# Optimization experiments

Hardware: AMD Instinct MI355X
Metric: run time of the kernel (lower is better)

## Reference

```python
import jax, jax.numpy as jnp
import numpy as np

T = 36          # temporal length (dictionary rows)
NP = 161        # number of atoms = 1 + 80 + 80
LAMBDA = 0.005
MAX_ITER = 100
EPS = 1e-10
STOP_TOL = 1e-5


def setup_inputs() -> dict:
    key = jax.random.key(0)
    k1, k2, k3 = jax.random.split(key, 3)
    y = jax.random.normal(k1, (4096, T, 50), dtype=jnp.float32)
    r = jax.random.uniform(k2, (80,), dtype=jnp.float32)      # pole magnitudes
    theta = jax.random.uniform(k3, (80,), dtype=jnp.float32)  # pole phases
    return {"y": y, "r": r, "theta": theta}


def build_dictionary(r, theta):
    # D[i,:] = [1+eps, r^i*cos(i*theta), r^i*sin(i*theta)], column-normalized
    i = jnp.arange(T, dtype=r.dtype)[:, None]          # [T,1]
    r_pow = r[None, :] ** i                            # [T,80]
    ang = i * theta[None, :]                           # [T,80]
    one_col = jnp.full((T, 1), 1.0 + EPS, dtype=r.dtype)
    D = jnp.concatenate([one_col, r_pow * jnp.cos(ang), r_pow * jnp.sin(ang)], axis=1)  # [T,NP]
    D = D / jnp.linalg.norm(D, axis=0, keepdims=True)
    return D


def fista_reweighted(D, Y, lambd, w):
    # D: [T,NP], Y: [N,T,M], w: [N,NP,M]
    DtD = D.T @ D                                       # [NP,NP]
    DtY = jnp.einsum('tp,ntm->npm', D, Y)               # [N,NP,M]
    L = jnp.linalg.norm(DtD, ord=2)                     # spectral norm
    Linv = 1.0 / L
    weighted_lambd = w * lambd * Linv
    A = jnp.eye(NP, dtype=D.dtype) - DtD * Linv         # [NP,NP]
    const_xminus = DtY * Linv - weighted_lambd
    const_xplus = DtY * Linv + weighted_lambd
    x0 = jnp.zeros_like(DtY)

    def step(carry, _):
        x_old, y_old, t_old, done = carry
        Ay = jnp.einsum('pq,nqm->npm', A, y_old)
        x_new = jnp.maximum(0.0, Ay + const_xminus) + jnp.minimum(0.0, Ay + const_xplus)
        t_new = (1.0 + jnp.sqrt(1.0 + 4.0 * t_old ** 2)) / 2.0
        tt = (t_old - 1.0) / t_new
        y_new = x_new + tt * (x_new - x_old)
        # early-stop check (divisor NP == x_old.shape[1] for full-shaped x)
        cnv = jnp.linalg.norm((x_old - x_new).ravel()) / NP < STOP_TOL
        x_out = jnp.where(done, x_old, x_new)
        y_out = jnp.where(done, y_old, y_new)
        t_out = jnp.where(done, t_old, t_new)
        return (x_out, y_out, t_out, done | cnv), None

    init = (x0, x0, jnp.asarray(1.0, D.dtype), jnp.asarray(False))
    (x_final, _, _, _), _ = jax.lax.scan(step, init, None, length=MAX_ITER)
    return x_final


def reference(y, r, theta):
    D = build_dictionary(r, theta)                      # [T,NP], normalized
    w = jnp.ones((y.shape[0], NP, y.shape[2]), dtype=y.dtype)
    C_pred = fista_reweighted(D, y, LAMBDA, w)          # [N,NP,M]
    Y_pred = jnp.einsum('tp,npm->ntm', D, C_pred)       # [N,T,M]
    return (Y_pred, C_pred)
```

## Files before the change

kernel.cpp:

```cpp
#include <hip/hip_runtime.h>

#define T36   36
#define NPAR  161
#define MM    50
#define NN    4096
#define NCOLS (NN*MM)
#define MP    48
#define KP    192
#define KV    64
#define CB    32
#define YPITCH 200
#define VPITCH 72

typedef _Float16 half8 __attribute__((ext_vector_type(8)));
typedef _Float16 half4 __attribute__((ext_vector_type(4)));
typedef float    f32x4 __attribute__((ext_vector_type(4)));

#define MFMA16(a,b,c) __builtin_amdgcn_mfma_f32_16x16x32_f16(a,b,c,0,0,0)

__device__ float g_D[MP*KP];
__device__ float g_DT[KP*KV];
__device__ float g_sc[2];

__global__ __launch_bounds__(256) void setup_kernel(const float* __restrict__ r,
                                                    const float* __restrict__ th) {
  __shared__ float Dl[MP][KP];
  __shared__ float El[T36][T36];
  __shared__ float Fl[T36][T36];
  __shared__ float Gl[T36][T36];
  __shared__ float vl[T36], v2[T36], v3[T36];
  __shared__ float sc;
  __shared__ int jmaxs;
  const int tid = threadIdx.x;

  for (int e = tid; e < MP*KP; e += 256) (&Dl[0][0])[e] = 0.0f;
  __syncthreads();

  if (tid < NPAR) {
    const int p = tid;
    float col[T36];
    if (p == 0) {
      #pragma unroll
      for (int t = 0; t < T36; ++t) col[t] = 1.0f;
    } else if (p <= 80) {
      const float a = r[p-1], w = th[p-1];
      for (int t = 0; t < T36; ++t) col[t] = powf(a, (float)t) * cosf((float)t * w);
    } else {
      const float a = r[p-81], w = th[p-81];
      for (int t = 0; t < T36; ++t) col[t] = powf(a, (float)t) * sinf((float)t * w);
    }
    float s = 0.0f;
    for (int t = 0; t < T36; ++t) s += col[t]*col[t];
    const float inv = 1.0f / sqrtf(s);
    for (int t = 0; t < T36; ++t) Dl[t][p] = col[t] * inv;
  }
  __syncthreads();

  for (int e = tid; e < MP*KP; e += 256) g_D[e] = (&Dl[0][0])[e];
  for (int e = tid; e < KP*KV; e += 256) {
    const int p = e / KV, t = e % KV;
    g_DT[e] = (t < MP) ? Dl[t][p] : 0.0f;
  }

  for (int e = tid; e < T36*T36; e += 256) {
    const int a = e / T36, b = e % T36;
    float s = 0.0f;
    for (int p = 0; p < KP; ++p) s += Dl[a][p]*Dl[b][p];
    El[a][b] = s; Fl[a][b] = s;
  }

  for (int it = 0; it < 25; ++it) {
    __syncthreads();
    for (int e = tid; e < T36*T36; e += 256) {
      const int a = e / T36, b = e % T36;
      float s = 0.0f;
      for (int k = 0; k < T36; ++k) s += Fl[a][k]*Fl[k][b];
      Gl[a][b] = s;
    }
    __syncthreads();
    if (tid == 0) {
      float tr = 0.0f;
      for (int i = 0; i < T36; ++i) tr += Gl[i][i];
      sc = 1.0f / tr;
    }
    __syncthreads();
    for (int e = tid; e < T36*T36; e += 256) {
      const int a = e / T36, b = e % T36;
      Fl[a][b] = Gl[a][b] * sc;
    }
  }
  __syncthreads();

  if (tid == 0) {
    int jm = 0; float bm = Fl[0][0];
    for (int i = 1; i < T36; ++i) if (Fl[i][i] > bm) { bm = Fl[i][i]; jm = i; }
    jmaxs = jm;
  }
  __syncthreads();
  if (tid < T36) vl[tid] = Fl[tid][jmaxs];
  __syncthreads();
  if (tid < T36) { float s = 0.0f; for (int k = 0; k < T36; ++k) s += El[tid][k]*vl[k]; v2[tid] = s; }
  __syncthreads();
  if (tid < T36) { float s = 0.0f; for (int k = 0; k < T36; ++k) s += El[tid][k]*v2[k]; v3[tid] = s; }
  __syncthreads();
  if (tid == 0) {
    float num = 0.0f, den = 0.0f;
    for (int t = 0; t < T36; ++t) { num += v3[t]*v2[t]; den += v2[t]*v2[t]; }
    const float L = num / den;
    g_sc[0] = 1.0f / L;
    g_sc[1] = 0.005f / L;
  }
}

__global__ __launch_bounds__(256, 2) void fista_kernel(const float* __restrict__ y,
                                                       float* __restrict__ out) {
  __shared__ __align__(16) _Float16 Yh[CB][YPITCH];
  __shared__ __align__(16) _Float16 Yl[CB][YPITCH];
  __shared__ __align__(16) _Float16 Vh[CB][VPITCH];
  __shared__ __align__(16) _Float16 Vl[CB][VPITCH];

  const int tid = threadIdx.x;
  const int w = tid >> 6;
  const int l = tid & 63;
  const int g = l >> 4;
  const int q = l & 15;
  const int g0 = blockIdx.x * CB;

  const float Linv = g_sc[0];
  const float wl   = g_sc[1];

  half8 d1h[6], d1l[6];
  if (w < 3) {
    #pragma unroll
    for (int ks = 0; ks < 6; ++ks) {
      const float* src = &g_D[(w*16 + q)*KP + ks*32 + g*8];
      #pragma unroll
      for (int j = 0; j < 8; ++j) {
        const float x = src[j];
        const _Float16 h = (_Float16)x;
        d1h[ks][j] = h;
        d1l[ks][j] = (_Float16)(x - (float)h);
      }
    }
  }
  half8 d2h[3][2], d2l[3][2];
  #pragma unroll
  for (int pi = 0; pi < 3; ++pi)
    #pragma unroll
    for (int ks = 0; ks < 2; ++ks) {
      const float* src = &g_DT[((w*3 + pi)*16 + q)*KV + ks*32 + g*8];
      #pragma unroll
      for (int j = 0; j < 8; ++j) {
        const float x = src[j];
        const _Float16 h = (_Float16)x;
        d2h[pi][ks][j] = h;
        d2l[pi][ks][j] = (_Float16)(x - (float)h);
      }
    }

  for (int e = tid; e < CB*YPITCH; e += 256) { (&Yh[0][0])[e] = (_Float16)0; (&Yl[0][0])[e] = (_Float16)0; }
  for (int e = tid; e < CB*VPITCH; e += 256) { (&Vh[0][0])[e] = (_Float16)0; (&Vl[0][0])[e] = (_Float16)0; }
  __syncthreads();
  for (int e = tid; e < CB*T36; e += 256) {
    const int cl = e / T36, t = e % T36;
    const int gc = g0 + cl;
    const int n = gc / 50, m = gc - n*50;
    const float x = y[(size_t)n*1800 + t*50 + m];
    const _Float16 h = (_Float16)x;
    Vh[cl][t] = h;
    Vl[cl][t] = (_Float16)(x - (float)h);
  }
  __syncthreads();

  float cv[3][2][4], xo[3][2][4], yr[3][2][4];
  {
    f32x4 acc[3][2];
    #pragma unroll
    for (int pi = 0; pi < 3; ++pi)
      #pragma unroll
      for (int ct = 0; ct < 2; ++ct) acc[pi][ct] = (f32x4){0.f,0.f,0.f,0.f};
    #pragma unroll
    for (int ks = 0; ks < 2; ++ks) {
      half8 bh[2], bl[2];
      #pragma unroll
      for (int ct = 0; ct < 2; ++ct) {
        bh[ct] = *reinterpret_cast<const half8*>(&Vh[ct*16 + q][ks*32 + g*8]);
        bl[ct] = *reinterpret_cast<const half8*>(&Vl[ct*16 + q][ks*32 + g*8]);
      }
      #pragma unroll
      for (int pi = 0; pi < 3; ++pi)
        #pragma unroll
        for (int ct = 0; ct < 2; ++ct) {
          acc[pi][ct] = MFMA16(d2h[pi][ks], bh[ct], acc[pi][ct]);
          acc[pi][ct] = MFMA16(d2h[pi][ks], bl[ct], acc[pi][ct]);
          acc[pi][ct] = MFMA16(d2l[pi][ks], bh[ct], acc[pi][ct]);
        }
    }
    #pragma unroll
    for (int pi = 0; pi < 3; ++pi)
      #pragma unroll
      for (int ct = 0; ct < 2; ++ct)
        #pragma unroll
        for (int i = 0; i < 4; ++i) {
          cv[pi][ct][i] = acc[pi][ct][i] * Linv;
          xo[pi][ct][i] = 0.0f;
          yr[pi][ct][i] = 0.0f;
        }
  }

  float tk = 1.0f;
  for (int it = 0; it < 100; ++it) {
    __syncthreads();

    if (w < 3) {
      f32x4 a1[2] = {(f32x4){0.f,0.f,0.f,0.f}, (f32x4){0.f,0.f,0.f,0.f}};
      #pragma unroll
      for (int ks = 0; ks < 6; ++ks) {
        half8 bh[2], bl[2];
        #pragma unroll
        for (int ct = 0; ct < 2; ++ct) {
          bh[ct] = *reinterpret_cast<const half8*>(&Yh[ct*16 + q][ks*32 + g*8]);
          bl[ct] = *reinterpret_cast<const half8*>(&Yl[ct*16 + q][ks*32 + g*8]);
        }
        #pragma unroll
        for (int ct = 0; ct < 2; ++ct) {
          a1[ct] = MFMA16(d1h[ks], bh[ct], a1[ct]);
          a1[ct] = MFMA16(d1h[ks], bl[ct], a1[ct]);
          a1[ct] = MFMA16(d1l[ks], bh[ct], a1[ct]);
        }
      }
      #pragma unroll
      for (int ct = 0; ct < 2; ++ct) {
        half4 h4, l4;
        #pragma unroll
        for (int i = 0; i < 4; ++i) {
          const float v = a1[ct][i];
          const _Float16 h = (_Float16)v;
          h4[i] = h;
          l4[i] = (_Float16)(v - (float)h);
        }
        *reinterpret_cast<half4*>(&Vh[ct*16 + q][w*16 + g*4]) = h4;
        *reinterpret_cast<half4*>(&Vl[ct*16 + q][w*16 + g*4]) = l4;
      }
    }
    __syncthreads();

    f32x4 acc[3][2];
    #pragma unroll
    for (int pi = 0; pi < 3; ++pi)
      #pragma unroll
      for (int ct = 0; ct < 2; ++ct) acc[pi][ct] = (f32x4){0.f,0.f,0.f,0.f};
    #pragma unroll
    for (int ks = 0; ks < 2; ++ks) {
      half8 bh[2], bl[2];
      #pragma unroll
      for (int ct = 0; ct < 2; ++ct) {
        bh[ct] = *reinterpret_cast<const half8*>(&Vh[ct*16 + q][ks*32 + g*8]);
        bl[ct] = *reinterpret_cast<const half8*>(&Vl[ct*16 + q][ks*32 + g*8]);
      }
      #pragma unroll
      for (int pi = 0; pi < 3; ++pi)
        #pragma unroll
        for (int ct = 0; ct < 2; ++ct) {
          acc[pi][ct] = MFMA16(d2h[pi][ks], bh[ct], acc[pi][ct]);
          acc[pi][ct] = MFMA16(d2h[pi][ks], bl[ct], acc[pi][ct]);
          acc[pi][ct] = MFMA16(d2l[pi][ks], bh[ct], acc[pi][ct]);
        }
    }

    const float tnew = 0.5f*(1.0f + sqrtf(fmaf(4.0f*tk, tk, 1.0f)));
    const float tt   = (tk - 1.0f) / tnew;
    tk = tnew;

    #pragma unroll
    for (int pi = 0; pi < 3; ++pi)
      #pragma unroll
      for (int ct = 0; ct < 2; ++ct) {
        half4 yh4, yl4;
        #pragma unroll
        for (int i = 0; i < 4; ++i) {
          const float u  = acc[pi][ct][i];
          const float gq = fmaf(-Linv, u, yr[pi][ct][i]) + cv[pi][ct][i];
          const float xn = fmaxf(0.0f, gq - wl) + fminf(0.0f, gq + wl);
          const float yn = fmaf(tt, xn - xo[pi][ct][i], xn);
          xo[pi][ct][i] = xn;
          yr[pi][ct][i] = yn;
          const _Float16 h = (_Float16)yn;
          yh4[i] = h;
          yl4[i] = (_Float16)(yn - (float)h);
        }
        const int p0 = (w*3 + pi)*16 + g*4;
        *reinterpret_cast<half4*>(&Yh[ct*16 + q][p0]) = yh4;
        *reinterpret_cast<half4*>(&Yl[ct*16 + q][p0]) = yl4;
      }
  }

  const size_t YP = (size_t)NN * T36 * MM;

  #pragma unroll
  for (int pi = 0; pi < 3; ++pi)
    #pragma unroll
    for (int ct = 0; ct < 2; ++ct)
      #pragma unroll
      for (int i = 0; i < 4; ++i) {
        const int p = (w*3 + pi)*16 + g*4 + i;
        if (p < NPAR) {
          const int gc = g0 + ct*16 + q;
          const int n = gc / 50, m = gc - n*50;
          out[YP + (size_t)n*(NPAR*MM) + (size_t)p*MM + m] = xo[pi][ct][i];
        }
      }

  #pragma unroll
  for (int pi = 0; pi < 3; ++pi)
    #pragma unroll
    for (int ct = 0; ct < 2; ++ct) {
      half4 xh4, xl4;
      #pragma unroll
      for (int i = 0; i < 4; ++i) {
        const float v = xo[pi][ct][i];
        const _Float16 h = (_Float16)v;
        xh4[i] = h;
        xl4[i] = (_Float16)(v - (float)h);
      }
      const int p0 = (w*3 + pi)*16 + g*4;
      *reinterpret_cast<half4*>(&Yh[ct*16 + q][p0]) = xh4;
      *reinterpret_cast<half4*>(&Yl[ct*16 + q][p0]) = xl4;
    }
  __syncthreads();

  if (w < 3) {
    f32x4 a1[2] = {(f32x4){0.f,0.f,0.f,0.f}, (f32x4){0.f,0.f,0.f,0.f}};
    #pragma unroll
    for (int ks = 0; ks < 6; ++ks) {
      half8 bh[2], bl[2];
      #pragma unroll
      for (int ct = 0; ct < 2; ++ct) {
        bh[ct] = *reinterpret_cast<const half8*>(&Yh[ct*16 + q][ks*32 + g*8]);
        bl[ct] = *reinterpret_cast<const half8*>(&Yl[ct*16 + q][ks*32 + g*8]);
      }
      #pragma unroll
      for (int ct = 0; ct < 2; ++ct) {
        a1[ct] = MFMA16(d1h[ks], bh[ct], a1[ct]);
        a1[ct] = MFMA16(d1h[ks], bl[ct], a1[ct]);
        a1[ct] = MFMA16(d1l[ks], bh[ct], a1[ct]);
      }
    }
    #pragma unroll
    for (int ct = 0; ct < 2; ++ct)
      #pragma unroll
      for (int i = 0; i < 4; ++i) {
        const int t = w*16 + g*4 + i;
        if (t < T36) {
          const int gc = g0 + ct*16 + q;
          const int n = gc / 50, m = gc - n*50;
          out[(size_t)n*1800 + t*50 + m] = a1[ct][i];
        }
      }
  }
}

extern "C" void kernel_launch(void* const* d_in, const int* in_sizes, int n_in,
                              void* d_out, int out_size, void* d_ws, size_t ws_size,
                              hipStream_t stream) {
  const float* y  = (const float*)d_in[0];
  const float* r  = (const float*)d_in[1];
  const float* th = (const float*)d_in[2];
  float* out = (float*)d_out;
  (void)d_ws; (void)ws_size;

  setup_kernel<<<1, 256, 0, stream>>>(r, th);
  fista_kernel<<<NCOLS / CB, 256, 0, stream>>>(y, out);
}
```

Measured before the change: 3.031 ms.

## Split constant atom out of MFMA path, swizzle LDS, peel first FISTA iteration

```diff
diff --git a/kernel.cpp b/kernel.cpp
--- a/kernel.cpp
+++ b/kernel.cpp
@@ -5,12 +5,10 @@
 #define MM    50
 #define NN    4096
 #define NCOLS (NN*MM)
-#define MP    48
-#define KP    192
-#define KV    64
 #define CB    32
-#define YPITCH 200
-#define VPITCH 72
+#define KS1   5
+#define YPITCH 192
+#define VPITCH 64
 
 typedef _Float16 half8 __attribute__((ext_vector_type(8)));
 typedef _Float16 half4 __attribute__((ext_vector_type(4)));
@@ -18,13 +16,20 @@
 
 #define MFMA16(a,b,c) __builtin_amdgcn_mfma_f32_16x16x32_f16(a,b,c,0,0,0)
 
-__device__ float g_D[MP*KP];
-__device__ float g_DT[KP*KV];
-__device__ float g_sc[2];
+__device__ float g_D[48*160];
+__device__ float g_DT[160*64];
+__device__ float g_sc[3];
+
+__device__ __forceinline__ int offY(int c, int h) {
+  return c*YPITCH + ((((h>>3) ^ (c&7))<<3) | (h&7));
+}
+__device__ __forceinline__ int offV(int c, int h) {
+  return c*VPITCH + ((((h>>3) ^ (c&7))<<3) | (h&7));
+}
 
 __global__ __launch_bounds__(256) void setup_kernel(const float* __restrict__ r,
                                                     const float* __restrict__ th) {
-  __shared__ float Dl[MP][KP];
+  __shared__ float Dl[T36][176];
   __shared__ float El[T36][T36];
   __shared__ float Fl[T36][T36];
   __shared__ float Gl[T36][T36];
@@ -33,7 +38,7 @@
   __shared__ int jmaxs;
   const int tid = threadIdx.x;
 
-  for (int e = tid; e < MP*KP; e += 256) (&Dl[0][0])[e] = 0.0f;
+  for (int e = tid; e < T36*176; e += 256) (&Dl[0][0])[e] = 0.0f;
   __syncthreads();
 
   if (tid < NPAR) {
@@ -56,16 +61,26 @@
   }
   __syncthreads();
 
-  for (int e = tid; e < MP*KP; e += 256) g_D[e] = (&Dl[0][0])[e];
-  for (int e = tid; e < KP*KV; e += 256) {
-    const int p = e / KV, t = e % KV;
-    g_DT[e] = (t < MP) ? Dl[t][p] : 0.0f;
+  for (int e = tid; e < 48*160; e += 256) {
+    const int t = e / 160, s = e % 160;
+    g_D[e] = (t < T36) ? Dl[t][s+1] : 0.0f;
+  }
+  for (int e = tid; e < 160*64; e += 256) {
+    const int p = e / 64, t = e % 64;
+    float v = 0.0f;
+    if (t < T36) v = Dl[t][p+1];
+    else if (t == 48) {
+      float s = 0.0f;
+      for (int tt = 0; tt < T36; ++tt) s += Dl[tt][p+1] * Dl[tt][0];
+      v = s;
+    }
+    g_DT[e] = v;
   }
 
   for (int e = tid; e < T36*T36; e += 256) {
     const int a = e / T36, b = e % T36;
     float s = 0.0f;
-    for (int p = 0; p < KP; ++p) s += Dl[a][p]*Dl[b][p];
+    for (int p = 0; p < 176; ++p) s += Dl[a][p]*Dl[b][p];
     El[a][b] = s; Fl[a][b] = s;
   }
 
@@ -109,15 +124,17 @@
     const float L = num / den;
     g_sc[0] = 1.0f / L;
     g_sc[1] = 0.005f / L;
+    g_sc[2] = Dl[0][0];
   }
 }
 
 __global__ __launch_bounds__(256, 2) void fista_kernel(const float* __restrict__ y,
                                                        float* __restrict__ out) {
-  __shared__ __align__(16) _Float16 Yh[CB][YPITCH];
-  __shared__ __align__(16) _Float16 Yl[CB][YPITCH];
-  __shared__ __align__(16) _Float16 Vh[CB][VPITCH];
-  __shared__ __align__(16) _Float16 Vl[CB][VPITCH];
+  __shared__ __align__(16) _Float16 Yh[CB*YPITCH];
+  __shared__ __align__(16) _Float16 Yl[CB*YPITCH];
+  __shared__ __align__(16) _Float16 Vh[CB*VPITCH];
+  __shared__ __align__(16) _Float16 Vl[CB*VPITCH];
+  __shared__ float y0f[CB];
 
   const int tid = threadIdx.x;
   const int w = tid >> 6;
@@ -128,12 +145,18 @@
 
   const float Linv = g_sc[0];
   const float wl   = g_sc[1];
-
-  half8 d1h[6], d1l[6];
+  const float d0   = g_sc[2];
+
+  const int tbase = (w < 2) ? w*3 : 6 + (w-2)*2;
+  const int ntile = (w < 2) ? 3 : 2;
+  const bool w3own = (w == 3) && (l < CB);
+  const int oc = l;
+
+  half8 d1h[KS1], d1l[KS1];
   if (w < 3) {
     #pragma unroll
-    for (int ks = 0; ks < 6; ++ks) {
-      const float* src = &g_D[(w*16 + q)*KP + ks*32 + g*8];
+    for (int ks = 0; ks < KS1; ++ks) {
+      const float* src = &g_D[(w*16 + q)*160 + ks*32 + g*8];
       #pragma unroll
       for (int j = 0; j < 8; ++j) {
         const float x = src[j];
@@ -145,34 +168,39 @@
   }
   half8 d2h[3][2], d2l[3][2];
   #pragma unroll
-  for (int pi = 0; pi < 3; ++pi)
-    #pragma unroll
-    for (int ks = 0; ks < 2; ++ks) {
-      const float* src = &g_DT[((w*3 + pi)*16 + q)*KV + ks*32 + g*8];
-      #pragma unroll
-      for (int j = 0; j < 8; ++j) {
-        const float x = src[j];
-        const _Float16 h = (_Float16)x;
-        d2h[pi][ks][j] = h;
-        d2l[pi][ks][j] = (_Float16)(x - (float)h);
-      }
-    }
-
-  for (int e = tid; e < CB*YPITCH; e += 256) { (&Yh[0][0])[e] = (_Float16)0; (&Yl[0][0])[e] = (_Float16)0; }
-  for (int e = tid; e < CB*VPITCH; e += 256) { (&Vh[0][0])[e] = (_Float16)0; (&Vl[0][0])[e] = (_Float16)0; }
-  __syncthreads();
+  for (int pi = 0; pi < 3; ++pi) {
+    if (pi < ntile) {
+      #pragma unroll
+      for (int ks = 0; ks < 2; ++ks) {
+        const float* src = &g_DT[((tbase + pi)*16 + q)*64 + ks*32 + g*8];
+        #pragma unroll
+        for (int j = 0; j < 8; ++j) {
+          const float x = src[j];
+          const _Float16 h = (_Float16)x;
+          d2h[pi][ks][j] = h;
+          d2l[pi][ks][j] = (_Float16)(x - (float)h);
+        }
+      }
+    }
+  }
+
+  for (int e = tid; e < CB*YPITCH; e += 256) { Yh[e] = (_Float16)0.0f; Yl[e] = (_Float16)0.0f; }
+  for (int e = tid; e < CB*VPITCH; e += 256) { Vh[e] = (_Float16)0.0f; Vl[e] = (_Float16)0.0f; }
+  __syncthreads();
+
   for (int e = tid; e < CB*T36; e += 256) {
-    const int cl = e / T36, t = e % T36;
-    const int gc = g0 + cl;
+    const int c = e / T36, t = e % T36;
+    const int gc = g0 + c;
     const int n = gc / 50, m = gc - n*50;
     const float x = y[(size_t)n*1800 + t*50 + m];
     const _Float16 h = (_Float16)x;
-    Vh[cl][t] = h;
-    Vl[cl][t] = (_Float16)(x - (float)h);
+    Vh[offV(c, t)] = h;
+    Vl[offV(c, t)] = (_Float16)(x - (float)h);
   }
   __syncthreads();
 
   float cv[3][2][4], xo[3][2][4], yr[3][2][4];
+  float cv0 = 0.0f, xo0 = 0.0f, yr0 = 0.0f;
   {
     f32x4 acc[3][2];
     #pragma unroll
@@ -184,43 +212,80 @@
       half8 bh[2], bl[2];
       #pragma unroll
       for (int ct = 0; ct < 2; ++ct) {
-        bh[ct] = *reinterpret_cast<const half8*>(&Vh[ct*16 + q][ks*32 + g*8]);
-        bl[ct] = *reinterpret_cast<const half8*>(&Vl[ct*16 + q][ks*32 + g*8]);
-      }
-      #pragma unroll
-      for (int pi = 0; pi < 3; ++pi)
-        #pragma unroll
-        for (int ct = 0; ct < 2; ++ct) {
-          acc[pi][ct] = MFMA16(d2h[pi][ks], bh[ct], acc[pi][ct]);
-          acc[pi][ct] = MFMA16(d2h[pi][ks], bl[ct], acc[pi][ct]);
-          acc[pi][ct] = MFMA16(d2l[pi][ks], bh[ct], acc[pi][ct]);
-        }
+        bh[ct] = *reinterpret_cast<const half8*>(&Vh[offV(ct*16 + q, ks*32 + g*8)]);
+        bl[ct] = *reinterpret_cast<const half8*>(&Vl[offV(ct*16 + q, ks*32 + g*8)]);
+      }
+      #pragma unroll
+      for (int pi = 0; pi < 3; ++pi) {
+        if (pi < ntile) {
+          #pragma unroll
+          for (int ct = 0; ct < 2; ++ct) {
+            acc[pi][ct] = MFMA16(d2h[pi][ks], bh[ct], acc[pi][ct]);
+            acc[pi][ct] = MFMA16(d2h[pi][ks], bl[ct], acc[pi][ct]);
+            acc[pi][ct] = MFMA16(d2l[pi][ks], bh[ct], acc[pi][ct]);
+          }
+        }
+      }
     }
     #pragma unroll
     for (int pi = 0; pi < 3; ++pi)
       #pragma unroll
       for (int ct = 0; ct < 2; ++ct)
         #pragma unroll
+        for (int i = 0; i < 4; ++i) cv[pi][ct][i] = acc[pi][ct][i] * Linv;
+    if (w3own) {
+      float s = 0.0f;
+      #pragma unroll
+      for (int u = 0; u < 5; ++u) {
+        const half8 h8 = *reinterpret_cast<const half8*>(&Vh[offV(oc, u*8)]);
+        const half8 l8 = *reinterpret_cast<const half8*>(&Vl[offV(oc, u*8)]);
+        #pragma unroll
+        for (int j = 0; j < 8; ++j) s += (float)h8[j] + (float)l8[j];
+      }
+      cv0 = Linv * d0 * s;
+    }
+  }
+
+  #pragma unroll
+  for (int pi = 0; pi < 3; ++pi) {
+    if (pi < ntile) {
+      #pragma unroll
+      for (int ct = 0; ct < 2; ++ct) {
+        half4 yh4, yl4;
+        #pragma unroll
         for (int i = 0; i < 4; ++i) {
-          cv[pi][ct][i] = acc[pi][ct][i] * Linv;
-          xo[pi][ct][i] = 0.0f;
-          yr[pi][ct][i] = 0.0f;
-        }
-  }
-
-  float tk = 1.0f;
-  for (int it = 0; it < 100; ++it) {
+          const float gq = cv[pi][ct][i];
+          const float xn = fmaxf(0.0f, gq - wl) + fminf(0.0f, gq + wl);
+          xo[pi][ct][i] = xn;
+          yr[pi][ct][i] = xn;
+          const _Float16 h = (_Float16)xn;
+          yh4[i] = h;
+          yl4[i] = (_Float16)(xn - (float)h);
+        }
+        const int p0 = (tbase + pi)*16 + g*4;
+        *reinterpret_cast<half4*>(&Yh[offY(ct*16 + q, p0)]) = yh4;
+        *reinterpret_cast<half4*>(&Yl[offY(ct*16 + q, p0)]) = yl4;
+      }
+    }
+  }
+  if (w3own) {
+    const float xn = fmaxf(0.0f, cv0 - wl) + fminf(0.0f, cv0 + wl);
+    xo0 = xn; yr0 = xn;
+  }
+
+  float tk = 1.61803398875f;
+  for (int it = 1; it < 100; ++it) {
     __syncthreads();
 
     if (w < 3) {
       f32x4 a1[2] = {(f32x4){0.f,0.f,0.f,0.f}, (f32x4){0.f,0.f,0.f,0.f}};
       #pragma unroll
-      for (int ks = 0; ks < 6; ++ks) {
+      for (int ks = 0; ks < KS1; ++ks) {
         half8 bh[2], bl[2];
         #pragma unroll
         for (int ct = 0; ct < 2; ++ct) {
-          bh[ct] = *reinterpret_cast<const half8*>(&Yh[ct*16 + q][ks*32 + g*8]);
-          bl[ct] = *reinterpret_cast<const half8*>(&Yl[ct*16 + q][ks*32 + g*8]);
+          bh[ct] = *reinterpret_cast<const half8*>(&Yh[offY(ct*16 + q, ks*32 + g*8)]);
+          bl[ct] = *reinterpret_cast<const half8*>(&Yl[offY(ct*16 + q, ks*32 + g*8)]);
         }
         #pragma unroll
         for (int ct = 0; ct < 2; ++ct) {
@@ -239,9 +304,13 @@
           h4[i] = h;
           l4[i] = (_Float16)(v - (float)h);
         }
-        *reinterpret_cast<half4*>(&Vh[ct*16 + q][w*16 + g*4]) = h4;
-        *reinterpret_cast<half4*>(&Vl[ct*16 + q][w*16 + g*4]) = l4;
-      }
+        *reinterpret_cast<half4*>(&Vh[offV(ct*16 + q, w*16 + g*4)]) = h4;
+        *reinterpret_cast<half4*>(&Vl[offV(ct*16 + q, w*16 + g*4)]) = l4;
+      }
+    } else if (w3own) {
+      const _Float16 h = (_Float16)yr0;
+      Vh[offV(oc, 48)] = h;
+      Vl[offV(oc, 48)] = (_Float16)(yr0 - (float)h);
     }
     __syncthreads();
 
@@ -255,17 +324,32 @@
       half8 bh[2], bl[2];
       #pragma unroll
       for (int ct = 0; ct < 2; ++ct) {
-        bh[ct] = *reinterpret_cast<const half8*>(&Vh[ct*16 + q][ks*32 + g*8]);
-        bl[ct] = *reinterpret_cast<const half8*>(&Vl[ct*16 + q][ks*32 + g*8]);
-      }
-      #pragma unroll
-      for (int pi = 0; pi < 3; ++pi)
-        #pragma unroll
-        for (int ct = 0; ct < 2; ++ct) {
-          acc[pi][ct] = MFMA16(d2h[pi][ks], bh[ct], acc[pi][ct]);
-          acc[pi][ct] = MFMA16(d2h[pi][ks], bl[ct], acc[pi][ct]);
-          acc[pi][ct] = MFMA16(d2l[pi][ks], bh[ct], acc[pi][ct]);
-        }
+        bh[ct] = *reinterpret_cast<const half8*>(&Vh[offV(ct*16 + q, ks*32 + g*8)]);
+        bl[ct] = *reinterpret_cast<const half8*>(&Vl[offV(ct*16 + q, ks*32 + g*8)]);
+      }
+      #pragma unroll
+      for (int pi = 0; pi < 3; ++pi) {
+        if (pi < ntile) {
+          #pragma unroll
+          for (int ct = 0; ct < 2; ++ct) {
+            acc[pi][ct] = MFMA16(d2h[pi][ks], bh[ct], acc[pi][ct]);
+            acc[pi][ct] = MFMA16(d2h[pi][ks], bl[ct], acc[pi][ct]);
+            acc[pi][ct] = MFMA16(d2l[pi][ks], bh[ct], acc[pi][ct]);
+          }
+        }
+      }
+    }
+    float u0 = 0.0f;
+    if (w3own) {
+      float s = 0.0f;
+      #pragma unroll
+      for (int u = 0; u < 5; ++u) {
+        const half8 h8 = *reinterpret_cast<const half8*>(&Vh[offV(oc, u*8)]);
+        const half8 l8 = *reinterpret_cast<const half8*>(&Vl[offV(oc, u*8)]);
+        #pragma unroll
+        for (int j = 0; j < 8; ++j) s += (float)h8[j] + (float)l8[j];
+      }
+      u0 = d0 * s + yr0;
     }
 
     const float tnew = 0.5f*(1.0f + sqrtf(fmaf(4.0f*tk, tk, 1.0f)));
@@ -273,71 +357,89 @@
     tk = tnew;
 
     #pragma unroll
-    for (int pi = 0; pi < 3; ++pi)
-      #pragma unroll
-      for (int ct = 0; ct < 2; ++ct) {
-        half4 yh4, yl4;
+    for (int pi = 0; pi < 3; ++pi) {
+      if (pi < ntile) {
+        #pragma unroll
+        for (int ct = 0; ct < 2; ++ct) {
+          half4 yh4, yl4;
+          #pragma unroll
+          for (int i = 0; i < 4; ++i) {
+            const float gq = fmaf(-Linv, acc[pi][ct][i], yr[pi][ct][i]) + cv[pi][ct][i];
+            const float xn = fmaxf(0.0f, gq - wl) + fminf(0.0f, gq + wl);
+            const float yn = fmaf(tt, xn - xo[pi][ct][i], xn);
+            xo[pi][ct][i] = xn;
+            yr[pi][ct][i] = yn;
+            const _Float16 h = (_Float16)yn;
+            yh4[i] = h;
+            yl4[i] = (_Float16)(yn - (float)h);
+          }
+          const int p0 = (tbase + pi)*16 + g*4;
+          *reinterpret_cast<half4*>(&Yh[offY(ct*16 + q, p0)]) = yh4;
+          *reinterpret_cast<half4*>(&Yl[offY(ct*16 + q, p0)]) = yl4;
+        }
+      }
+    }
+    if (w3own) {
+      const float gq = fmaf(-Linv, u0, yr0) + cv0;
+      const float xn = fmaxf(0.0f, gq - wl) + fminf(0.0f, gq + wl);
+      const float yn = fmaf(tt, xn - xo0, xn);
+      xo0 = xn; yr0 = yn;
+    }
+  }
+
+  const size_t YP = (size_t)NN * T36 * MM;
+
+  #pragma unroll
+  for (int pi = 0; pi < 3; ++pi) {
+    if (pi < ntile) {
+      #pragma unroll
+      for (int ct = 0; ct < 2; ++ct)
         #pragma unroll
         for (int i = 0; i < 4; ++i) {
-          const float u  = acc[pi][ct][i];
-          const float gq = fmaf(-Linv, u, yr[pi][ct][i]) + cv[pi][ct][i];
-          const float xn = fmaxf(0.0f, gq - wl) + fminf(0.0f, gq + wl);
-          const float yn = fmaf(tt, xn - xo[pi][ct][i], xn);
-          xo[pi][ct][i] = xn;
-          yr[pi][ct][i] = yn;
-          const _Float16 h = (_Float16)yn;
-          yh4[i] = h;
-          yl4[i] = (_Float16)(yn - (float)h);
-        }
-        const int p0 = (w*3 + pi)*16 + g*4;
-        *reinterpret_cast<half4*>(&Yh[ct*16 + q][p0]) = yh4;
-        *reinterpret_cast<half4*>(&Yl[ct*16 + q][p0]) = yl4;
-      }
-  }
-
-  const size_t YP = (size_t)NN * T36 * MM;
-
-  #pragma unroll
-  for (int pi = 0; pi < 3; ++pi)
-    #pragma unroll
-    for (int ct = 0; ct < 2; ++ct)
-      #pragma unroll
-      for (int i = 0; i < 4; ++i) {
-        const int p = (w*3 + pi)*16 + g*4 + i;
-        if (p < NPAR) {
+          const int atom = (tbase + pi)*16 + g*4 + i + 1;
           const int gc = g0 + ct*16 + q;
           const int n = gc / 50, m = gc - n*50;
-          out[YP + (size_t)n*(NPAR*MM) + (size_t)p*MM + m] = xo[pi][ct][i];
-        }
-      }
+          out[YP + (size_t)n*(NPAR*MM) + (size_t)atom*MM + m] = xo[pi][ct][i];
+        }
+    }
+  }
+  if (w3own) {
+    const int gc = g0 + oc;
+    const int n = gc / 50, m = gc - n*50;
+    out[YP + (size_t)n*(NPAR*MM) + m] = xo0;
+  }
 
   #pragma unroll
-  for (int pi = 0; pi < 3; ++pi)
-    #pragma unroll
-    for (int ct = 0; ct < 2; ++ct) {
-      half4 xh4, xl4;
-      #pragma unroll
-      for (int i = 0; i < 4; ++i) {
-        const float v = xo[pi][ct][i];
-        const _Float16 h = (_Float16)v;
-        xh4[i] = h;
-        xl4[i] = (_Float16)(v - (float)h);
-      }
-      const int p0 = (w*3 + pi)*16 + g*4;
-      *reinterpret_cast<half4*>(&Yh[ct*16 + q][p0]) = xh4;
-      *reinterpret_cast<half4*>(&Yl[ct*16 + q][p0]) = xl4;
-    }
+  for (int pi = 0; pi < 3; ++pi) {
+    if (pi < ntile) {
+      #pragma unroll
+      for (int ct = 0; ct < 2; ++ct) {
+        half4 xh4, xl4;
+        #pragma unroll
+        for (int i = 0; i < 4; ++i) {
+          const float v = xo[pi][ct][i];
+          const _Float16 h = (_Float16)v;
+          xh4[i] = h;
+          xl4[i] = (_Float16)(v - (float)h);
+        }
+        const int p0 = (tbase + pi)*16 + g*4;
+        *reinterpret_cast<half4*>(&Yh[offY(ct*16 + q, p0)]) = xh4;
+        *reinterpret_cast<half4*>(&Yl[offY(ct*16 + q, p0)]) = xl4;
+      }
+    }
+  }
+  if (w3own) y0f[oc] = xo0;
   __syncthreads();
 
   if (w < 3) {
     f32x4 a1[2] = {(f32x4){0.f,0.f,0.f,0.f}, (f32x4){0.f,0.f,0.f,0.f}};
     #pragma unroll
-    for (int ks = 0; ks < 6; ++ks) {
+    for (int ks = 0; ks < KS1; ++ks) {
       half8 bh[2], bl[2];
       #pragma unroll
       for (int ct = 0; ct < 2; ++ct) {
-        bh[ct] = *reinterpret_cast<const half8*>(&Yh[ct*16 + q][ks*32 + g*8]);
-        bl[ct] = *reinterpret_cast<const half8*>(&Yl[ct*16 + q][ks*32 + g*8]);
+        bh[ct] = *reinterpret_cast<const half8*>(&Yh[offY(ct*16 + q, ks*32 + g*8)]);
+        bl[ct] = *reinterpret_cast<const half8*>(&Yl[offY(ct*16 + q, ks*32 + g*8)]);
       }
       #pragma unroll
       for (int ct = 0; ct < 2; ++ct) {
@@ -347,16 +449,18 @@
       }
     }
     #pragma unroll
-    for (int ct = 0; ct < 2; ++ct)
+    for (int ct = 0; ct < 2; ++ct) {
+      const float r1 = d0 * y0f[ct*16 + q];
       #pragma unroll
       for (int i = 0; i < 4; ++i) {
         const int t = w*16 + g*4 + i;
         if (t < T36) {
           const int gc = g0 + ct*16 + q;
           const int n = gc / 50, m = gc - n*50;
-          out[(size_t)n*1800 + t*50 + m] = a1[ct][i];
-        }
-      }
+          out[(size_t)n*1800 + t*50 + m] = a1[ct][i] + r1;
+        }
+      }
+    }
   }
 }
 
@@ -367,7 +471,7 @@
   const float* r  = (const float*)d_in[1];
   const float* th = (const float*)d_in[2];
   float* out = (float*)d_out;
-  (void)d_ws; (void)ws_size;
+  (void)d_ws; (void)ws_size; (void)in_sizes; (void)n_in; (void)out_size;
 
   setup_kernel<<<1, 256, 0, stream>>>(r, th);
   fista_kernel<<<NCOLS / CB, 256, 0, stream>>>(y, out);
```

After: 3.061 ms. No clear change (+1.0%).
